# Kernel tuning notes

Hardware: AMD Instinct MI355X
Metric: run time of the kernel (lower is better)

## Reference

```python
import jax, jax.numpy as jnp
import numpy as np

N = 100000
F = 256
H = 128
C = 64
E = 1600000

def spmm(rows, cols, vals, h):
    # sparse [N,N] @ dense [N,D] via gather + segment-sum
    return jax.ops.segment_sum(vals[:, None] * h[cols], rows, num_segments=N)

def graph_conv(x, W, rows, cols, vals, b=None):
    # GraphConv: support = x @ W; out = adj @ support (+ bias)
    out = spmm(rows, cols, vals, x @ W)
    if b is not None:
        out = out + b
    return out

def setup_inputs() -> dict:
    key = jax.random.key(0)
    ks = jax.random.split(key, 20)
    d = {}
    d['x'] = jax.random.normal(ks[0], (N, F), dtype=jnp.float32)
    for i, name in enumerate(['mid', 'low', 'high']):
        d[name + '_rows'] = jax.random.randint(ks[1 + 3 * i], (E,), 0, N, dtype=jnp.int64 if jax.config.jax_enable_x64 else jnp.int32)
        d[name + '_cols'] = jax.random.randint(ks[2 + 3 * i], (E,), 0, N, dtype=jnp.int64 if jax.config.jax_enable_x64 else jnp.int32)
        d[name + '_vals'] = jax.random.uniform(ks[3 + 3 * i], (E,), dtype=jnp.float32) * 0.1
    s = lambda k, a, b_: jax.random.normal(k, (a, b_), dtype=jnp.float32) * (1.0 / np.sqrt(a))
    d['W_hid'] = s(ks[10], F, H)          # hidden_layers[0], no bias
    d['W_out'] = s(ks[11], H, C)          # out_layer
    d['b_out'] = jnp.zeros((C,), jnp.float32)
    d['W_low'] = s(ks[12], F, H)          # addHid_layer, no bias
    d['W_low_out'] = s(ks[13], H, C)      # addOut_layer
    d['b_low_out'] = jnp.zeros((C,), jnp.float32)
    d['W_high'] = s(ks[14], F, H)         # addHid_layer_HIGH, no bias
    d['W_high_out'] = s(ks[15], H, C)     # addOut_layer_HIGH
    d['b_high_out'] = jnp.zeros((C,), jnp.float32)
    d['gate2'] = jnp.array([0.5], jnp.float32)
    return d

def reference(x, mid_rows, mid_cols, mid_vals, low_rows, low_cols, low_vals,
              high_rows, high_cols, high_vals, W_hid, W_out, b_out,
              W_low, W_low_out, b_low_out, W_high, W_high_out, b_high_out, gate2):
    # dropout is identity at inference
    h = jax.nn.relu(graph_conv(x, W_hid, mid_rows, mid_cols, mid_vals))
    h = graph_conv(h, W_out, mid_rows, mid_cols, mid_vals, b_out)
    x2 = jax.nn.relu(graph_conv(x, W_low, low_rows, low_cols, low_vals))
    xh = jax.nn.relu(graph_conv(x, W_high, high_rows, high_cols, high_vals))
    x2 = graph_conv(x2, W_low_out, low_rows, low_cols, low_vals, b_low_out)
    xh = graph_conv(xh, W_high_out, high_rows, high_cols, high_vals, b_high_out)
    x_final = gate2 * h + (1.0 - gate2) * (x2 + xh)
    return jax.nn.log_softmax(x_final, axis=-1)
```

## Files before the change

### kernel.cpp

```cpp
#include <hip/hip_runtime.h>
#include <math.h>

#define NNODES 100000
#define NEDGES 1600000
#define FEAT 256
#define HID 128
#define NCLS 64
#define RPB 512
#define NBG 196
#define NB3 (3 * NBG)
#define CAP 8832
#define SC_CHUNK 8192
#define SC_THREADS 1024

typedef __attribute__((ext_vector_type(8))) short bf16x8;
typedef __attribute__((ext_vector_type(4))) float f32x4;

__device__ __forceinline__ float bf2f(unsigned int u16) {
  union { unsigned int i; float f; } c; c.i = u16 << 16; return c.f;
}
__device__ __forceinline__ unsigned short f2bf(float f) {
  union { float f; unsigned int i; } c; c.f = f;
  unsigned int u = c.i;
  return (unsigned short)((u + 0x7fffu + ((u >> 16) & 1u)) >> 16);
}

__global__ __launch_bounds__(256) void k_bhist(const int* __restrict__ r0,
                                               const int* __restrict__ r1,
                                               const int* __restrict__ r2,
                                               int* __restrict__ bhist) {
  __shared__ int h[NBG];
  int g = blockIdx.y;
  const int* rr = (g == 0) ? r0 : (g == 1 ? r1 : r2);
  int tid = threadIdx.x;
  for (int i = tid; i < NBG; i += 256) h[i] = 0;
  __syncthreads();
  int base = blockIdx.x * 4096;
#pragma unroll
  for (int k = 0; k < 16; k++) {
    int e = base + k * 256 + tid;
    if (e < NEDGES) atomicAdd(&h[rr[e] >> 9], 1);
  }
  __syncthreads();
  for (int i = tid; i < NBG; i += 256)
    if (h[i]) atomicAdd(&bhist[g * NBG + i], h[i]);
}

__global__ __launch_bounds__(1024) void k_bscan(const int* __restrict__ bhist,
                                                int* __restrict__ boff) {
  __shared__ int sd[2][1024];
  int tid = threadIdx.x;
  int v = (tid < NB3) ? bhist[tid] : 0;
  sd[0][tid] = v;
  __syncthreads();
  int cur = 0;
  for (int off = 1; off < 1024; off <<= 1) {
    int nv = sd[cur][tid];
    if (tid >= off) nv += sd[cur][tid - off];
    sd[cur ^ 1][tid] = nv;
    __syncthreads();
    cur ^= 1;
  }
  int incl = sd[cur][tid];
  if (tid < NB3) boff[tid] = incl - v;
  if (tid == NB3 - 1) boff[NB3] = incl;
}

__global__ __launch_bounds__(SC_THREADS) void k_bucket_scatter(
    const int* __restrict__ r0, const int* __restrict__ r1, const int* __restrict__ r2,
    const int* __restrict__ c0, const int* __restrict__ c1, const int* __restrict__ c2,
    const float* __restrict__ v0, const float* __restrict__ v1, const float* __restrict__ v2,
    int* __restrict__ gcur, int2* __restrict__ edges) {
  __shared__ int2 stage[SC_CHUNK];
  __shared__ unsigned char bid[SC_CHUNK];
  __shared__ int hist[NBG];
  __shared__ int lbase[NBG];
  __shared__ int gstart[NBG];
  __shared__ int cur[NBG];
  __shared__ int sd[2][256];
  int g = blockIdx.y;
  const int*   rr = (g == 0) ? r0 : (g == 1 ? r1 : r2);
  const int*   cc = (g == 0) ? c0 : (g == 1 ? c1 : c2);
  const float* vv = (g == 0) ? v0 : (g == 1 ? v1 : v2);
  int tid = threadIdx.x;
  int base = blockIdx.x * SC_CHUNK;
  int cnt_blk = NEDGES - base;
  if (cnt_blk > SC_CHUNK) cnt_blk = SC_CHUNK;

  for (int i = tid; i < NBG; i += SC_THREADS) hist[i] = 0;
  __syncthreads();

  int rowv[SC_CHUNK / SC_THREADS];
  int colv[SC_CHUNK / SC_THREADS];
  float valv[SC_CHUNK / SC_THREADS];
#pragma unroll
  for (int k = 0; k < SC_CHUNK / SC_THREADS; k++) {
    int e = base + k * SC_THREADS + tid;
    bool ok = e < NEDGES;
    rowv[k] = ok ? rr[e] : -1;
    colv[k] = ok ? cc[e] : 0;
    valv[k] = ok ? vv[e] : 0.f;
    if (ok) atomicAdd(&hist[rowv[k] >> 9], 1);
  }
  __syncthreads();

  if (tid < 256) sd[0][tid] = (tid < NBG) ? hist[tid] : 0;
  __syncthreads();
  int c = 0;
  for (int off = 1; off < 256; off <<= 1) {
    if (tid < 256) {
      int nv = sd[c][tid];
      if (tid >= off) nv += sd[c][tid - off];
      sd[c ^ 1][tid] = nv;
    }
    __syncthreads();
    c ^= 1;
  }
  if (tid < NBG) {
    int cn = hist[tid];
    int excl = sd[c][tid] - cn;
    lbase[tid] = excl;
    cur[tid] = excl;
    gstart[tid] = cn ? atomicAdd(&gcur[g * NBG + tid], cn) : 0;
  }
  __syncthreads();

#pragma unroll
  for (int k = 0; k < SC_CHUNK / SC_THREADS; k++) {
    if (rowv[k] >= 0) {
      int b = rowv[k] >> 9;
      int p = atomicAdd(&cur[b], 1);
      stage[p] = make_int2(((rowv[k] & (RPB - 1)) << 17) | colv[k], __float_as_int(valv[k]));
      bid[p] = (unsigned char)b;
    }
  }
  __syncthreads();

  for (int i = tid; i < cnt_blk; i += SC_THREADS) {
    int b = bid[i];
    int dst = gstart[b] + (i - lbase[b]);
    edges[dst] = stage[i];
  }
}

__global__ __launch_bounds__(512) void k_bucket_sort(const int* __restrict__ boff,
                                                     int2* __restrict__ edges,
                                                     int* __restrict__ row_ptr_all) {
  __shared__ int2 stage[CAP];
  __shared__ int hist[RPB];
  __shared__ int sd[2][RPB];
  __shared__ int cur[RPB];
  int g = blockIdx.y, b = blockIdx.x;
  int tid = threadIdx.x;
  int idx = g * NBG + b;
  int base = boff[idx];
  int count = boff[idx + 1] - base;
  if (count > CAP) count = CAP;
  hist[tid] = 0;
  __syncthreads();

  const int KSL = (CAP + 511) / 512;
  int2 ev[KSL];
#pragma unroll
  for (int k = 0; k < KSL; k++) {
    int i = tid + k * 512;
    if (i < count) {
      ev[k] = edges[base + i];
      atomicAdd(&hist[ev[k].x >> 17], 1);
    }
  }
  __syncthreads();

  int v = hist[tid];
  sd[0][tid] = v;
  __syncthreads();
  int c2 = 0;
  for (int off = 1; off < 512; off <<= 1) {
    int nv = sd[c2][tid];
    if (tid >= off) nv += sd[c2][tid - off];
    sd[c2 ^ 1][tid] = nv;
    __syncthreads();
    c2 ^= 1;
  }
  int excl = sd[c2][tid] - v;
  int row = b * RPB + tid;
  if (row <= NNODES) row_ptr_all[g * (NNODES + 1) + row] = base + excl;
  cur[tid] = excl;
  __syncthreads();

#pragma unroll
  for (int k = 0; k < KSL; k++) {
    int i = tid + k * 512;
    if (i < count) {
      int lr = ev[k].x >> 17;
      int p = atomicAdd(&cur[lr], 1);
      stage[p] = make_int2(ev[k].x & 0x1FFFF, ev[k].y);
    }
  }
  __syncthreads();

  for (int i = tid; i < count; i += 512) edges[base + i] = stage[i];
}

__global__ __launch_bounds__(256) void k_convert_bf16(const float* __restrict__ src,
                                                      unsigned short* __restrict__ dst,
                                                      int n4) {
  int i = blockIdx.x * blockDim.x + threadIdx.x;
  if (i < n4) {
    float4 v = ((const float4*)src)[i];
    ushort4 o;
    o.x = f2bf(v.x); o.y = f2bf(v.y); o.z = f2bf(v.z); o.w = f2bf(v.w);
    ((ushort4*)dst)[i] = o;
  }
}

__global__ __launch_bounds__(256) void k_transpose3(const float* __restrict__ s0,
                                                    const float* __restrict__ s1,
                                                    const float* __restrict__ s2,
                                                    unsigned short* __restrict__ d0,
                                                    unsigned short* __restrict__ d1,
                                                    unsigned short* __restrict__ d2,
                                                    int K, int N) {
  int g = blockIdx.y;
  const float* src = (g == 0) ? s0 : (g == 1 ? s1 : s2);
  unsigned short* dst = (g == 0) ? d0 : (g == 1 ? d1 : d2);
  int idx = blockIdx.x * 256 + threadIdx.x;
  if (idx < K * N) {
    int k = idx / N, n = idx % N;
    dst[(size_t)n * K + k] = f2bf(src[idx]);
  }
}

__global__ __launch_bounds__(256) void k_gemm1(const unsigned short* __restrict__ A,
                                               const unsigned short* __restrict__ Wt,
                                               unsigned short* __restrict__ C, int M) {
  int tid = threadIdx.x;
  int wave = tid >> 6, lane = tid & 63;
  int quad = lane >> 4, r = lane & 15;
  int m0 = blockIdx.x * 128 + wave * 32;
  int ra0 = m0 + r;      if (ra0 >= M) ra0 = 0;
  int ra1 = m0 + 16 + r; if (ra1 >= M) ra1 = 0;
  const unsigned short* pa0 = A + (size_t)ra0 * FEAT + quad * 8;
  const unsigned short* pa1 = A + (size_t)ra1 * FEAT + quad * 8;
  f32x4 acc[2][8];
#pragma unroll
  for (int i = 0; i < 2; i++)
#pragma unroll
    for (int j = 0; j < 8; j++) acc[i][j] = (f32x4){0.f, 0.f, 0.f, 0.f};
  for (int k0 = 0; k0 < FEAT; k0 += 32) {
    bf16x8 a0 = *(const bf16x8*)(pa0 + k0);
    bf16x8 a1 = *(const bf16x8*)(pa1 + k0);
#pragma unroll
    for (int nt = 0; nt < 8; nt++) {
      bf16x8 b = *(const bf16x8*)(Wt + (size_t)(nt * 16 + r) * FEAT + k0 + quad * 8);
      acc[0][nt] = __builtin_amdgcn_mfma_f32_16x16x32_bf16(a0, b, acc[0][nt], 0, 0, 0);
      acc[1][nt] = __builtin_amdgcn_mfma_f32_16x16x32_bf16(a1, b, acc[1][nt], 0, 0, 0);
    }
  }
#pragma unroll
  for (int t = 0; t < 2; t++)
#pragma unroll
    for (int reg = 0; reg < 4; reg++) {
      int row = m0 + t * 16 + quad * 4 + reg;
      if (row < M) {
#pragma unroll
        for (int nt = 0; nt < 8; nt++)
          C[(size_t)row * HID + nt * 16 + r] = f2bf(acc[t][nt][reg]);
      }
    }
}

__global__ __launch_bounds__(256) void k_gemm2(const unsigned short* __restrict__ A,
                                               const unsigned short* __restrict__ Wt,
                                               unsigned short* __restrict__ C, int M) {
  int tid = threadIdx.x;
  int wave = tid >> 6, lane = tid & 63;
  int quad = lane >> 4, r = lane & 15;
  int m0 = blockIdx.x * 128 + wave * 32;
  int ra0 = m0 + r;      if (ra0 >= M) ra0 = 0;
  int ra1 = m0 + 16 + r; if (ra1 >= M) ra1 = 0;
  const unsigned short* pa0 = A + (size_t)ra0 * HID + quad * 8;
  const unsigned short* pa1 = A + (size_t)ra1 * HID + quad * 8;
  f32x4 acc[2][4];
#pragma unroll
  for (int i = 0; i < 2; i++)
#pragma unroll
    for (int j = 0; j < 4; j++) acc[i][j] = (f32x4){0.f, 0.f, 0.f, 0.f};
  for (int k0 = 0; k0 < HID; k0 += 32) {
    bf16x8 a0 = *(const bf16x8*)(pa0 + k0);
    bf16x8 a1 = *(const bf16x8*)(pa1 + k0);
#pragma unroll
    for (int nt = 0; nt < 4; nt++) {
      bf16x8 b = *(const bf16x8*)(Wt + (size_t)(nt * 16 + r) * HID + k0 + quad * 8);
      acc[0][nt] = __builtin_amdgcn_mfma_f32_16x16x32_bf16(a0, b, acc[0][nt], 0, 0, 0);
      acc[1][nt] = __builtin_amdgcn_mfma_f32_16x16x32_bf16(a1, b, acc[1][nt], 0, 0, 0);
    }
  }
#pragma unroll
  for (int t = 0; t < 2; t++)
#pragma unroll
    for (int reg = 0; reg < 4; reg++) {
      int row = m0 + t * 16 + quad * 4 + reg;
      if (row < M) {
#pragma unroll
        for (int nt = 0; nt < 4; nt++)
          C[(size_t)row * NCLS + nt * 16 + r] = f2bf(acc[t][nt][reg]);
      }
    }
}

__global__ __launch_bounds__(256) void k_spmm128_relu(const int* __restrict__ rp,
                                                      const int2* __restrict__ edges,
                                                      const unsigned short* __restrict__ dense,
                                                      unsigned short* __restrict__ out, int n) {
  int w = (blockIdx.x * blockDim.x + threadIdx.x) >> 6;
  int lane = threadIdx.x & 63;
  if (w >= n) return;
  int grp = lane >> 4;
  int sub = lane & 15;
  int s = rp[w], e = rp[w + 1];
  float acc[8];
#pragma unroll
  for (int i = 0; i < 8; i++) acc[i] = 0.f;
  for (int j = s; j < e; j += 4) {
    int ej = j + grp;
    bool valid = ej < e;
    int2 ed = edges[valid ? ej : s];
    float v = valid ? __int_as_float(ed.y) : 0.f;
    bf16x8 u = *(const bf16x8*)(dense + (size_t)ed.x * 128 + sub * 8);
#pragma unroll
    for (int i = 0; i < 8; i++)
      acc[i] = fmaf(v, bf2f((unsigned short)u[i]), acc[i]);
  }
#pragma unroll
  for (int i = 0; i < 8; i++) {
    acc[i] += __shfl_xor(acc[i], 32, 64);
    acc[i] += __shfl_xor(acc[i], 16, 64);
    acc[i] = fmaxf(acc[i], 0.f);
  }
  if (lane < 16) {
    uint4 pk;
    pk.x = (unsigned int)f2bf(acc[0]) | ((unsigned int)f2bf(acc[1]) << 16);
    pk.y = (unsigned int)f2bf(acc[2]) | ((unsigned int)f2bf(acc[3]) << 16);
    pk.z = (unsigned int)f2bf(acc[4]) | ((unsigned int)f2bf(acc[5]) << 16);
    pk.w = (unsigned int)f2bf(acc[6]) | ((unsigned int)f2bf(acc[7]) << 16);
    *(uint4*)(out + (size_t)w * 128 + sub * 8) = pk;
  }
}

__global__ __launch_bounds__(256) void k_spmm64_gate(const int* __restrict__ rp,
                                                     const int2* __restrict__ edges,
                                                     const unsigned short* __restrict__ dense,
                                                     const float* __restrict__ bias,
                                                     const float* __restrict__ gate,
                                                     float* __restrict__ logits,
                                                     float* __restrict__ final_out,
                                                     int n, int mode, int one_minus) {
  int w = (blockIdx.x * blockDim.x + threadIdx.x) >> 6;
  int lane = threadIdx.x & 63;
  if (w >= n) return;
  int grp = lane >> 3;
  int sub = lane & 7;
  int s = rp[w], e = rp[w + 1];
  float acc[8];
#pragma unroll
  for (int i = 0; i < 8; i++) acc[i] = 0.f;
  for (int j = s; j < e; j += 8) {
    int ej = j + grp;
    bool valid = ej < e;
    int2 ed = edges[valid ? ej : s];
    float v = valid ? __int_as_float(ed.y) : 0.f;
    bf16x8 u = *(const bf16x8*)(dense + (size_t)ed.x * 64 + sub * 8);
#pragma unroll
    for (int i = 0; i < 8; i++)
      acc[i] = fmaf(v, bf2f((unsigned short)u[i]), acc[i]);
  }
#pragma unroll
  for (int i = 0; i < 8; i++) {
    acc[i] += __shfl_xor(acc[i], 32, 64);
    acc[i] += __shfl_xor(acc[i], 16, 64);
    acc[i] += __shfl_xor(acc[i], 8, 64);
  }
  float gv = gate[0];
  float scale = one_minus ? (1.0f - gv) : gv;
  float4 b0 = *(const float4*)(bias + sub * 8);
  float4 b1 = *(const float4*)(bias + sub * 8 + 4);
  float vc[8];
  vc[0] = scale * (acc[0] + b0.x); vc[1] = scale * (acc[1] + b0.y);
  vc[2] = scale * (acc[2] + b0.z); vc[3] = scale * (acc[3] + b0.w);
  vc[4] = scale * (acc[4] + b1.x); vc[5] = scale * (acc[5] + b1.y);
  vc[6] = scale * (acc[6] + b1.z); vc[7] = scale * (acc[7] + b1.w);
  size_t o = (size_t)w * 64 + sub * 8;
  if (mode == 0) {
    if (grp == 0) {
      *(float4*)(logits + o)     = make_float4(vc[0], vc[1], vc[2], vc[3]);
      *(float4*)(logits + o + 4) = make_float4(vc[4], vc[5], vc[6], vc[7]);
    }
  } else if (mode == 1) {
    float4 L0 = *(const float4*)(logits + o);
    float4 L1 = *(const float4*)(logits + o + 4);
    if (grp == 0) {
      *(float4*)(logits + o)     = make_float4(vc[0] + L0.x, vc[1] + L0.y, vc[2] + L0.z, vc[3] + L0.w);
      *(float4*)(logits + o + 4) = make_float4(vc[4] + L1.x, vc[5] + L1.y, vc[6] + L1.z, vc[7] + L1.w);
    }
  } else {
    float4 L0 = *(const float4*)(logits + o);
    float4 L1 = *(const float4*)(logits + o + 4);
    vc[0] += L0.x; vc[1] += L0.y; vc[2] += L0.z; vc[3] += L0.w;
    vc[4] += L1.x; vc[5] += L1.y; vc[6] += L1.z; vc[7] += L1.w;
    float m = vc[0];
#pragma unroll
    for (int i = 1; i < 8; i++) m = fmaxf(m, vc[i]);
    m = fmaxf(m, __shfl_xor(m, 1, 64));
    m = fmaxf(m, __shfl_xor(m, 2, 64));
    m = fmaxf(m, __shfl_xor(m, 4, 64));
    float sum = 0.f;
#pragma unroll
    for (int i = 0; i < 8; i++) sum += expf(vc[i] - m);
    sum += __shfl_xor(sum, 1, 64);
    sum += __shfl_xor(sum, 2, 64);
    sum += __shfl_xor(sum, 4, 64);
    float ls = m + logf(sum);
    if (grp == 0) {
      *(float4*)(final_out + o)     = make_float4(vc[0] - ls, vc[1] - ls, vc[2] - ls, vc[3] - ls);
      *(float4*)(final_out + o + 4) = make_float4(vc[4] - ls, vc[5] - ls, vc[6] - ls, vc[7] - ls);
    }
  }
}

extern "C" void kernel_launch(void* const* d_in, const int* in_sizes, int n_in,
                              void* d_out, int out_size, void* d_ws, size_t ws_size,
                              hipStream_t stream) {
  (void)in_sizes; (void)n_in; (void)out_size; (void)ws_size;
  const float* x = (const float*)d_in[0];
  const int*   rows[3]   = {(const int*)d_in[1], (const int*)d_in[4], (const int*)d_in[7]};
  const int*   colsIn[3] = {(const int*)d_in[2], (const int*)d_in[5], (const int*)d_in[8]};
  const float* valsIn[3] = {(const float*)d_in[3], (const float*)d_in[6], (const float*)d_in[9]};
  const float* Whid[3] = {(const float*)d_in[10], (const float*)d_in[13], (const float*)d_in[16]};
  const float* Wout[3] = {(const float*)d_in[11], (const float*)d_in[14], (const float*)d_in[17]};
  const float* bout[3] = {(const float*)d_in[12], (const float*)d_in[15], (const float*)d_in[18]};
  const float* gate = (const float*)d_in[19];
  float* out = (float*)d_out;

  const int N = NNODES, E = NEDGES;
  size_t off = 0;
  auto ws = [&](size_t bytes) {
    void* p = (char*)d_ws + off;
    off += (bytes + 255) & ~(size_t)255;
    return p;
  };
  unsigned short* x_bf = (unsigned short*)ws((size_t)N * FEAT * 2);
  unsigned short* Wt1[3], *Wt2[3];
  for (int g = 0; g < 3; g++) Wt1[g] = (unsigned short*)ws((size_t)HID * FEAT * 2);
  for (int g = 0; g < 3; g++) Wt2[g] = (unsigned short*)ws((size_t)NCLS * HID * 2);
  unsigned short* hsup   = (unsigned short*)ws((size_t)N * HID * 2);
  unsigned short* h1     = (unsigned short*)ws((size_t)N * HID * 2);
  float*          logits = (float*)         ws((size_t)N * NCLS * 4);
  unsigned short* h2     = hsup;
  int2* edges   = (int2*)ws((size_t)3 * E * 8);
  int*  rp_all  = (int*) ws((size_t)3 * (N + 1) * 4);
  int*  bhist   = (int*) ws(NB3 * 4);
  int*  boff    = (int*) ws((NB3 + 1) * 4);
  int*  gcur    = (int*) ws(NB3 * 4);

  dim3 b256(256);
  dim3 gRows((N + 3) / 4);
  dim3 gGemm((N + 127) / 128);

  k_convert_bf16<<<(N * FEAT / 4 + 255) / 256, b256, 0, stream>>>(x, x_bf, N * FEAT / 4);
  k_transpose3<<<dim3((FEAT * HID + 255) / 256, 3), b256, 0, stream>>>(
      Whid[0], Whid[1], Whid[2], Wt1[0], Wt1[1], Wt1[2], FEAT, HID);
  k_transpose3<<<dim3((HID * NCLS + 255) / 256, 3), b256, 0, stream>>>(
      Wout[0], Wout[1], Wout[2], Wt2[0], Wt2[1], Wt2[2], HID, NCLS);

  hipMemsetAsync(bhist, 0, NB3 * 4, stream);
  k_bhist<<<dim3((E + 4095) / 4096, 3), b256, 0, stream>>>(rows[0], rows[1], rows[2], bhist);
  k_bscan<<<1, 1024, 0, stream>>>(bhist, boff);
  hipMemcpyAsync(gcur, boff, NB3 * 4, hipMemcpyDeviceToDevice, stream);
  k_bucket_scatter<<<dim3((E + SC_CHUNK - 1) / SC_CHUNK, 3), dim3(SC_THREADS), 0, stream>>>(
      rows[0], rows[1], rows[2], colsIn[0], colsIn[1], colsIn[2],
      valsIn[0], valsIn[1], valsIn[2], gcur, edges);
  k_bucket_sort<<<dim3(NBG, 3), 512, 0, stream>>>(boff, edges, rp_all);

  for (int g = 0; g < 3; g++) {
    const int* rp = rp_all + (size_t)g * (N + 1);
    k_gemm1<<<gGemm, b256, 0, stream>>>(x_bf, Wt1[g], hsup, N);
    k_spmm128_relu<<<gRows, b256, 0, stream>>>(rp, edges, hsup, h1, N);
    k_gemm2<<<gGemm, b256, 0, stream>>>(h1, Wt2[g], h2, N);
    k_spmm64_gate<<<gRows, b256, 0, stream>>>(rp, edges, h2, bout[g], gate, logits, out, N,
                                              g, (g != 0));
  }
}
```

Before: 844.1 us.

## Batch three graph branches into single launches and unroll SpMM edge loop

The per-branch loop of four kernels is replaced by batched kernels that process all three adjacency branches in one launch through a grid dimension. The mid/low/high outputs go to separate logits buffers, and a new final kernel sums them and applies log-softmax. The SpMM inner loops now handle two edges per lane group per iteration with packed float2 FMAs, which raises memory-level parallelism. The batching is meant to cut launch overhead and fill the GPU better, at the cost of a larger workspace and an extra pass over the logits, with buffers aliased across stages.

```diff
diff --git a/kernel.cpp b/kernel.cpp
--- a/kernel.cpp
+++ b/kernel.cpp
@@ -15,6 +15,7 @@
 
 typedef __attribute__((ext_vector_type(8))) short bf16x8;
 typedef __attribute__((ext_vector_type(4))) float f32x4;
+typedef __attribute__((ext_vector_type(2))) float f32x2;
 
 __device__ __forceinline__ float bf2f(unsigned int u16) {
   union { unsigned int i; float f; } c; c.i = u16 << 16; return c.f;
@@ -23,6 +24,15 @@
   union { float f; unsigned int i; } c; c.f = f;
   unsigned int u = c.i;
   return (unsigned short)((u + 0x7fffu + ((u >> 16) & 1u)) >> 16);
+}
+
+__device__ __forceinline__ void fma8(const uint4 u, const f32x2 vv, f32x2* a) {
+  f32x2 p0, p1, p2, p3;
+  p0.x = __uint_as_float(u.x << 16); p0.y = __uint_as_float(u.x & 0xffff0000u);
+  p1.x = __uint_as_float(u.y << 16); p1.y = __uint_as_float(u.y & 0xffff0000u);
+  p2.x = __uint_as_float(u.z << 16); p2.y = __uint_as_float(u.z & 0xffff0000u);
+  p3.x = __uint_as_float(u.w << 16); p3.y = __uint_as_float(u.w & 0xffff0000u);
+  a[0] += p0 * vv; a[1] += p1 * vv; a[2] += p2 * vv; a[3] += p3 * vv;
 }
 
 __global__ __launch_bounds__(256) void k_bhist(const int* __restrict__ r0,
@@ -231,13 +241,18 @@
   }
 }
 
-__global__ __launch_bounds__(256) void k_gemm1(const unsigned short* __restrict__ A,
-                                               const unsigned short* __restrict__ Wt,
-                                               unsigned short* __restrict__ C, int M) {
+__global__ __launch_bounds__(256) void k_gemm1_b(const unsigned short* __restrict__ A,
+                                                 const unsigned short* __restrict__ WtA,
+                                                 unsigned short* __restrict__ C3, int M) {
+  int bxy = blockIdx.x;
+  int g = bxy % 3;
+  int bx = bxy / 3;
+  const unsigned short* Wt = WtA + (size_t)g * HID * FEAT;
+  unsigned short* C = C3 + (size_t)g * M * HID;
   int tid = threadIdx.x;
   int wave = tid >> 6, lane = tid & 63;
   int quad = lane >> 4, r = lane & 15;
-  int m0 = blockIdx.x * 128 + wave * 32;
+  int m0 = bx * 128 + wave * 32;
   int ra0 = m0 + r;      if (ra0 >= M) ra0 = 0;
   int ra1 = m0 + 16 + r; if (ra1 >= M) ra1 = 0;
   const unsigned short* pa0 = A + (size_t)ra0 * FEAT + quad * 8;
@@ -270,9 +285,13 @@
     }
 }
 
-__global__ __launch_bounds__(256) void k_gemm2(const unsigned short* __restrict__ A,
-                                               const unsigned short* __restrict__ Wt,
-                                               unsigned short* __restrict__ C, int M) {
+__global__ __launch_bounds__(256) void k_gemm2_b(const unsigned short* __restrict__ A3,
+                                                 const unsigned short* __restrict__ WtA,
+                                                 unsigned short* __restrict__ C3, int M) {
+  int g = blockIdx.y;
+  const unsigned short* A = A3 + (size_t)g * M * HID;
+  const unsigned short* Wt = WtA + (size_t)g * NCLS * HID;
+  unsigned short* C = C3 + (size_t)g * M * NCLS;
   int tid = threadIdx.x;
   int wave = tid >> 6, lane = tid & 63;
   int quad = lane >> 4, r = lane & 15;
@@ -309,123 +328,143 @@
     }
 }
 
-__global__ __launch_bounds__(256) void k_spmm128_relu(const int* __restrict__ rp,
-                                                      const int2* __restrict__ edges,
-                                                      const unsigned short* __restrict__ dense,
-                                                      unsigned short* __restrict__ out, int n) {
+__global__ __launch_bounds__(256) void k_spmm128_b(const int* __restrict__ rp_all,
+                                                   const int2* __restrict__ edges,
+                                                   const unsigned short* __restrict__ dense3,
+                                                   unsigned short* __restrict__ out3, int n) {
+  int g = blockIdx.y;
+  const int* rp = rp_all + (size_t)g * (NNODES + 1);
+  const unsigned short* dense = dense3 + (size_t)g * NNODES * HID;
+  unsigned short* out = out3 + (size_t)g * NNODES * HID;
   int w = (blockIdx.x * blockDim.x + threadIdx.x) >> 6;
   int lane = threadIdx.x & 63;
   if (w >= n) return;
   int grp = lane >> 4;
   int sub = lane & 15;
   int s = rp[w], e = rp[w + 1];
-  float acc[8];
-#pragma unroll
-  for (int i = 0; i < 8; i++) acc[i] = 0.f;
-  for (int j = s; j < e; j += 4) {
-    int ej = j + grp;
-    bool valid = ej < e;
-    int2 ed = edges[valid ? ej : s];
-    float v = valid ? __int_as_float(ed.y) : 0.f;
-    bf16x8 u = *(const bf16x8*)(dense + (size_t)ed.x * 128 + sub * 8);
-#pragma unroll
-    for (int i = 0; i < 8; i++)
-      acc[i] = fmaf(v, bf2f((unsigned short)u[i]), acc[i]);
-  }
-#pragma unroll
-  for (int i = 0; i < 8; i++) {
-    acc[i] += __shfl_xor(acc[i], 32, 64);
-    acc[i] += __shfl_xor(acc[i], 16, 64);
-    acc[i] = fmaxf(acc[i], 0.f);
+  f32x2 a0[4], a1[4];
+#pragma unroll
+  for (int q = 0; q < 4; q++) { a0[q] = (f32x2){0.f, 0.f}; a1[q] = (f32x2){0.f, 0.f}; }
+  for (int j = s; j < e; j += 8) {
+    int e0 = j + grp, e1 = j + 4 + grp;
+    bool k0 = e0 < e, k1 = e1 < e;
+    int2 d0 = edges[k0 ? e0 : s];
+    int2 d1 = edges[k1 ? e1 : s];
+    uint4 u0 = *(const uint4*)(dense + (size_t)d0.x * HID + sub * 8);
+    uint4 u1 = *(const uint4*)(dense + (size_t)d1.x * HID + sub * 8);
+    float f0 = k0 ? __int_as_float(d0.y) : 0.f;
+    float f1 = k1 ? __int_as_float(d1.y) : 0.f;
+    f32x2 v0; v0.x = f0; v0.y = f0;
+    f32x2 v1; v1.x = f1; v1.y = f1;
+    fma8(u0, v0, a0);
+    fma8(u1, v1, a1);
+  }
+  unsigned int pk[4];
+#pragma unroll
+  for (int q = 0; q < 4; q++) {
+    float lo = a0[q].x + a1[q].x;
+    float hi = a0[q].y + a1[q].y;
+    lo += __shfl_xor(lo, 32, 64); lo += __shfl_xor(lo, 16, 64);
+    hi += __shfl_xor(hi, 32, 64); hi += __shfl_xor(hi, 16, 64);
+    lo = fmaxf(lo, 0.f); hi = fmaxf(hi, 0.f);
+    pk[q] = (unsigned int)f2bf(lo) | ((unsigned int)f2bf(hi) << 16);
   }
   if (lane < 16) {
-    uint4 pk;
-    pk.x = (unsigned int)f2bf(acc[0]) | ((unsigned int)f2bf(acc[1]) << 16);
-    pk.y = (unsigned int)f2bf(acc[2]) | ((unsigned int)f2bf(acc[3]) << 16);
-    pk.z = (unsigned int)f2bf(acc[4]) | ((unsigned int)f2bf(acc[5]) << 16);
-    pk.w = (unsigned int)f2bf(acc[6]) | ((unsigned int)f2bf(acc[7]) << 16);
-    *(uint4*)(out + (size_t)w * 128 + sub * 8) = pk;
-  }
-}
-
-__global__ __launch_bounds__(256) void k_spmm64_gate(const int* __restrict__ rp,
-                                                     const int2* __restrict__ edges,
-                                                     const unsigned short* __restrict__ dense,
-                                                     const float* __restrict__ bias,
-                                                     const float* __restrict__ gate,
-                                                     float* __restrict__ logits,
-                                                     float* __restrict__ final_out,
-                                                     int n, int mode, int one_minus) {
+    uint4 o; o.x = pk[0]; o.y = pk[1]; o.z = pk[2]; o.w = pk[3];
+    *(uint4*)(out + (size_t)w * HID + sub * 8) = o;
+  }
+}
+
+__global__ __launch_bounds__(256) void k_spmm64_b(const int* __restrict__ rp_all,
+                                                  const int2* __restrict__ edges,
+                                                  const unsigned short* __restrict__ dense3,
+                                                  const float* __restrict__ b0p,
+                                                  const float* __restrict__ b1p,
+                                                  const float* __restrict__ b2p,
+                                                  const float* __restrict__ gate,
+                                                  float* __restrict__ logits3, int n) {
+  int g = blockIdx.y;
+  const int* rp = rp_all + (size_t)g * (NNODES + 1);
+  const unsigned short* dense = dense3 + (size_t)g * NNODES * NCLS;
+  const float* bias = (g == 0) ? b0p : (g == 1 ? b1p : b2p);
+  float* logits = logits3 + (size_t)g * NNODES * NCLS;
   int w = (blockIdx.x * blockDim.x + threadIdx.x) >> 6;
   int lane = threadIdx.x & 63;
   if (w >= n) return;
   int grp = lane >> 3;
   int sub = lane & 7;
   int s = rp[w], e = rp[w + 1];
-  float acc[8];
-#pragma unroll
-  for (int i = 0; i < 8; i++) acc[i] = 0.f;
-  for (int j = s; j < e; j += 8) {
-    int ej = j + grp;
-    bool valid = ej < e;
-    int2 ed = edges[valid ? ej : s];
-    float v = valid ? __int_as_float(ed.y) : 0.f;
-    bf16x8 u = *(const bf16x8*)(dense + (size_t)ed.x * 64 + sub * 8);
-#pragma unroll
-    for (int i = 0; i < 8; i++)
-      acc[i] = fmaf(v, bf2f((unsigned short)u[i]), acc[i]);
-  }
-#pragma unroll
-  for (int i = 0; i < 8; i++) {
-    acc[i] += __shfl_xor(acc[i], 32, 64);
-    acc[i] += __shfl_xor(acc[i], 16, 64);
-    acc[i] += __shfl_xor(acc[i], 8, 64);
+  f32x2 a0[4], a1[4];
+#pragma unroll
+  for (int q = 0; q < 4; q++) { a0[q] = (f32x2){0.f, 0.f}; a1[q] = (f32x2){0.f, 0.f}; }
+  for (int j = s; j < e; j += 16) {
+    int e0 = j + grp, e1 = j + 8 + grp;
+    bool k0 = e0 < e, k1 = e1 < e;
+    int2 d0 = edges[k0 ? e0 : s];
+    int2 d1 = edges[k1 ? e1 : s];
+    uint4 u0 = *(const uint4*)(dense + (size_t)d0.x * NCLS + sub * 8);
+    uint4 u1 = *(const uint4*)(dense + (size_t)d1.x * NCLS + sub * 8);
+    float f0 = k0 ? __int_as_float(d0.y) : 0.f;
+    float f1 = k1 ? __int_as_float(d1.y) : 0.f;
+    f32x2 v0; v0.x = f0; v0.y = f0;
+    f32x2 v1; v1.x = f1; v1.y = f1;
+    fma8(u0, v0, a0);
+    fma8(u1, v1, a1);
   }
   float gv = gate[0];
-  float scale = one_minus ? (1.0f - gv) : gv;
-  float4 b0 = *(const float4*)(bias + sub * 8);
-  float4 b1 = *(const float4*)(bias + sub * 8 + 4);
+  float scale = (g == 0) ? gv : (1.0f - gv);
   float vc[8];
-  vc[0] = scale * (acc[0] + b0.x); vc[1] = scale * (acc[1] + b0.y);
-  vc[2] = scale * (acc[2] + b0.z); vc[3] = scale * (acc[3] + b0.w);
-  vc[4] = scale * (acc[4] + b1.x); vc[5] = scale * (acc[5] + b1.y);
-  vc[6] = scale * (acc[6] + b1.z); vc[7] = scale * (acc[7] + b1.w);
-  size_t o = (size_t)w * 64 + sub * 8;
-  if (mode == 0) {
-    if (grp == 0) {
-      *(float4*)(logits + o)     = make_float4(vc[0], vc[1], vc[2], vc[3]);
-      *(float4*)(logits + o + 4) = make_float4(vc[4], vc[5], vc[6], vc[7]);
-    }
-  } else if (mode == 1) {
-    float4 L0 = *(const float4*)(logits + o);
-    float4 L1 = *(const float4*)(logits + o + 4);
-    if (grp == 0) {
-      *(float4*)(logits + o)     = make_float4(vc[0] + L0.x, vc[1] + L0.y, vc[2] + L0.z, vc[3] + L0.w);
-      *(float4*)(logits + o + 4) = make_float4(vc[4] + L1.x, vc[5] + L1.y, vc[6] + L1.z, vc[7] + L1.w);
-    }
-  } else {
-    float4 L0 = *(const float4*)(logits + o);
-    float4 L1 = *(const float4*)(logits + o + 4);
-    vc[0] += L0.x; vc[1] += L0.y; vc[2] += L0.z; vc[3] += L0.w;
-    vc[4] += L1.x; vc[5] += L1.y; vc[6] += L1.z; vc[7] += L1.w;
-    float m = vc[0];
-#pragma unroll
-    for (int i = 1; i < 8; i++) m = fmaxf(m, vc[i]);
-    m = fmaxf(m, __shfl_xor(m, 1, 64));
-    m = fmaxf(m, __shfl_xor(m, 2, 64));
-    m = fmaxf(m, __shfl_xor(m, 4, 64));
-    float sum = 0.f;
-#pragma unroll
-    for (int i = 0; i < 8; i++) sum += expf(vc[i] - m);
-    sum += __shfl_xor(sum, 1, 64);
-    sum += __shfl_xor(sum, 2, 64);
-    sum += __shfl_xor(sum, 4, 64);
-    float ls = m + logf(sum);
-    if (grp == 0) {
-      *(float4*)(final_out + o)     = make_float4(vc[0] - ls, vc[1] - ls, vc[2] - ls, vc[3] - ls);
-      *(float4*)(final_out + o + 4) = make_float4(vc[4] - ls, vc[5] - ls, vc[6] - ls, vc[7] - ls);
-    }
-  }
+#pragma unroll
+  for (int q = 0; q < 4; q++) {
+    float lo = a0[q].x + a1[q].x;
+    float hi = a0[q].y + a1[q].y;
+    lo += __shfl_xor(lo, 32, 64); lo += __shfl_xor(lo, 16, 64); lo += __shfl_xor(lo, 8, 64);
+    hi += __shfl_xor(hi, 32, 64); hi += __shfl_xor(hi, 16, 64); hi += __shfl_xor(hi, 8, 64);
+    vc[2 * q] = lo; vc[2 * q + 1] = hi;
+  }
+  if (grp == 0) {
+    float4 b0 = *(const float4*)(bias + sub * 8);
+    float4 b1 = *(const float4*)(bias + sub * 8 + 4);
+    size_t o = (size_t)w * NCLS + sub * 8;
+    *(float4*)(logits + o) = make_float4(scale * (vc[0] + b0.x), scale * (vc[1] + b0.y),
+                                         scale * (vc[2] + b0.z), scale * (vc[3] + b0.w));
+    *(float4*)(logits + o + 4) = make_float4(scale * (vc[4] + b1.x), scale * (vc[5] + b1.y),
+                                             scale * (vc[6] + b1.z), scale * (vc[7] + b1.w));
+  }
+}
+
+__global__ __launch_bounds__(256) void k_final(const float* __restrict__ l3,
+                                               float* __restrict__ outp, int n) {
+  int t = blockIdx.x * 256 + threadIdx.x;
+  int w = t >> 3, sub = t & 7;
+  if (w >= n) return;
+  size_t o = (size_t)w * NCLS + sub * 8;
+  const float* p0 = l3 + o;
+  const float* p1 = l3 + (size_t)NNODES * NCLS + o;
+  const float* p2 = l3 + (size_t)2 * NNODES * NCLS + o;
+  float4 x0 = *(const float4*)p0, x1 = *(const float4*)(p0 + 4);
+  float4 y0 = *(const float4*)p1, y1 = *(const float4*)(p1 + 4);
+  float4 z0 = *(const float4*)p2, z1 = *(const float4*)(p2 + 4);
+  float v[8];
+  v[0] = x0.x + y0.x + z0.x; v[1] = x0.y + y0.y + z0.y;
+  v[2] = x0.z + y0.z + z0.z; v[3] = x0.w + y0.w + z0.w;
+  v[4] = x1.x + y1.x + z1.x; v[5] = x1.y + y1.y + z1.y;
+  v[6] = x1.z + y1.z + z1.z; v[7] = x1.w + y1.w + z1.w;
+  float m = v[0];
+#pragma unroll
+  for (int i = 1; i < 8; i++) m = fmaxf(m, v[i]);
+  m = fmaxf(m, __shfl_xor(m, 1, 64));
+  m = fmaxf(m, __shfl_xor(m, 2, 64));
+  m = fmaxf(m, __shfl_xor(m, 4, 64));
+  float sum = 0.f;
+#pragma unroll
+  for (int i = 0; i < 8; i++) sum += expf(v[i] - m);
+  sum += __shfl_xor(sum, 1, 64);
+  sum += __shfl_xor(sum, 2, 64);
+  sum += __shfl_xor(sum, 4, 64);
+  float ls = m + logf(sum);
+  *(float4*)(outp + o)     = make_float4(v[0] - ls, v[1] - ls, v[2] - ls, v[3] - ls);
+  *(float4*)(outp + o + 4) = make_float4(v[4] - ls, v[5] - ls, v[6] - ls, v[7] - ls);
 }
 
 extern "C" void kernel_launch(void* const* d_in, const int* in_sizes, int n_in,
@@ -449,14 +488,13 @@
     off += (bytes + 255) & ~(size_t)255;
     return p;
   };
-  unsigned short* x_bf = (unsigned short*)ws((size_t)N * FEAT * 2);
-  unsigned short* Wt1[3], *Wt2[3];
-  for (int g = 0; g < 3; g++) Wt1[g] = (unsigned short*)ws((size_t)HID * FEAT * 2);
-  for (int g = 0; g < 3; g++) Wt2[g] = (unsigned short*)ws((size_t)NCLS * HID * 2);
-  unsigned short* hsup   = (unsigned short*)ws((size_t)N * HID * 2);
-  unsigned short* h1     = (unsigned short*)ws((size_t)N * HID * 2);
-  float*          logits = (float*)         ws((size_t)N * NCLS * 4);
-  unsigned short* h2     = hsup;
+  unsigned short* R1 = (unsigned short*)ws((size_t)3 * N * HID * 2);
+  unsigned short* x_bf = R1;
+  unsigned short* h13  = R1;
+  float*          logits3 = (float*)R1;
+  unsigned short* hsup3 = (unsigned short*)ws((size_t)3 * N * HID * 2);
+  unsigned short* Wt1a = (unsigned short*)ws((size_t)3 * HID * FEAT * 2);
+  unsigned short* Wt2a = (unsigned short*)ws((size_t)3 * NCLS * HID * 2);
   int2* edges   = (int2*)ws((size_t)3 * E * 8);
   int*  rp_all  = (int*) ws((size_t)3 * (N + 1) * 4);
   int*  bhist   = (int*) ws(NB3 * 4);
@@ -464,14 +502,16 @@
   int*  gcur    = (int*) ws(NB3 * 4);
 
   dim3 b256(256);
-  dim3 gRows((N + 3) / 4);
-  dim3 gGemm((N + 127) / 128);
+  dim3 gRows3((N + 3) / 4, 3);
+  int nbGemm = (N + 127) / 128;
 
   k_convert_bf16<<<(N * FEAT / 4 + 255) / 256, b256, 0, stream>>>(x, x_bf, N * FEAT / 4);
   k_transpose3<<<dim3((FEAT * HID + 255) / 256, 3), b256, 0, stream>>>(
-      Whid[0], Whid[1], Whid[2], Wt1[0], Wt1[1], Wt1[2], FEAT, HID);
+      Whid[0], Whid[1], Whid[2], Wt1a, Wt1a + (size_t)HID * FEAT, Wt1a + (size_t)2 * HID * FEAT,
+      FEAT, HID);
   k_transpose3<<<dim3((HID * NCLS + 255) / 256, 3), b256, 0, stream>>>(
-      Wout[0], Wout[1], Wout[2], Wt2[0], Wt2[1], Wt2[2], HID, NCLS);
+      Wout[0], Wout[1], Wout[2], Wt2a, Wt2a + (size_t)NCLS * HID, Wt2a + (size_t)2 * NCLS * HID,
+      HID, NCLS);
 
   hipMemsetAsync(bhist, 0, NB3 * 4, stream);
   k_bhist<<<dim3((E + 4095) / 4096, 3), b256, 0, stream>>>(rows[0], rows[1], rows[2], bhist);
@@ -482,12 +522,10 @@
       valsIn[0], valsIn[1], valsIn[2], gcur, edges);
   k_bucket_sort<<<dim3(NBG, 3), 512, 0, stream>>>(boff, edges, rp_all);
 
-  for (int g = 0; g < 3; g++) {
-    const int* rp = rp_all + (size_t)g * (N + 1);
-    k_gemm1<<<gGemm, b256, 0, stream>>>(x_bf, Wt1[g], hsup, N);
-    k_spmm128_relu<<<gRows, b256, 0, stream>>>(rp, edges, hsup, h1, N);
-    k_gemm2<<<gGemm, b256, 0, stream>>>(h1, Wt2[g], h2, N);
-    k_spmm64_gate<<<gRows, b256, 0, stream>>>(rp, edges, h2, bout[g], gate, logits, out, N,
-                                              g, (g != 0));
-  }
-}
+  k_gemm1_b<<<dim3(3 * nbGemm), b256, 0, stream>>>(x_bf, Wt1a, hsup3, N);
+  k_spmm128_b<<<gRows3, b256, 0, stream>>>(rp_all, edges, hsup3, h13, N);
+  k_gemm2_b<<<dim3(nbGemm, 3), b256, 0, stream>>>(h13, Wt2a, hsup3, N);
+  k_spmm64_b<<<gRows3, b256, 0, stream>>>(rp_all, edges, hsup3, bout[0], bout[1], bout[2],
+                                          gate, logits3, N);
+  k_final<<<(N * 8 + 255) / 256, b256, 0, stream>>>(logits3, out, N);
+}
```

Result: faster. 727.6 us (-13.8%).
